# Optimization experiments

Measured on AMD Instinct MI355X. Metric: run time of the kernel, lower is better.

## Reference

```python
import jax, jax.numpy as jnp
import numpy as np

DIM = 2048
H = 16
HD = DIM // H  # 128
EPS = 1e-6


def _rmsnorm(x, w):
    # x: [b, s, d] (float32 math, matches torch RMSNorm .float())
    return x * jax.lax.rsqrt(jnp.mean(x * x, axis=-1, keepdims=True) + EPS) * w


def _rope(x, freqs):
    # x: [b, s, d]; freqs: [s, HD//2, 2] (real, imag) -- complex multiply per pair
    b, s, d = x.shape
    xp = x.reshape(b, s, H, HD // 2, 2)
    xr, xi = xp[..., 0], xp[..., 1]
    fr = freqs[None, :, None, :, 0]
    fi = freqs[None, :, None, :, 1]
    out = jnp.stack([xr * fr - xi * fi, xr * fi + xi * fr], axis=-1)
    return out.reshape(b, s, d)


def _attn(q, k, v):
    # q: [b, sq, d], k/v: [b, skv, d] -> standard SDPA over H heads
    b, sq, d = q.shape
    skv = k.shape[1]
    qh = q.reshape(b, sq, H, HD)
    kh = k.reshape(b, skv, H, HD)
    vh = v.reshape(b, skv, H, HD)
    scores = jnp.einsum('bqhd,bkhd->bhqk', qh, kh) / np.sqrt(HD).astype(np.float32)
    p = jax.nn.softmax(scores, axis=-1)
    out = jnp.einsum('bhqk,bkhd->bqhd', p, vh)
    return out.reshape(b, sq, d)


def _linear(x, w, bias):
    # torch Linear convention: w [out, in]
    return jnp.einsum('bsi,oi->bso', x, w) + bias


def setup_inputs() -> dict:
    key = jax.random.key(0)
    ks = jax.random.split(key, 24)
    rn = lambda k, sh, s=1.0: jax.random.normal(k, sh, dtype=jnp.float32) * s
    B, SX, SC, SR = 2, 2048, 512, 512
    W = 0.02
    return {
        'x': rn(ks[0], (B, SX, DIM)),
        'cam_emb': rn(ks[1], (B, SC, DIM)),
        'render_emb': rn(ks[2], (B, SR, DIM)),
        'freqs_x': rn(ks[3], (SX, HD // 2, 2)),
        'freqs_cam': rn(ks[4], (SC, HD // 2, 2)),
        'freqs_render': rn(ks[5], (SR, HD // 2, 2)),
        'wq': rn(ks[6], (DIM, DIM), W), 'bq': jnp.zeros((DIM,), jnp.float32),
        'wk': rn(ks[7], (DIM, DIM), W), 'bk': jnp.zeros((DIM,), jnp.float32),
        'wv': rn(ks[8], (DIM, DIM), W), 'bv': jnp.zeros((DIM,), jnp.float32),
        'wkr': rn(ks[9], (DIM, DIM), W), 'bkr': jnp.zeros((DIM,), jnp.float32),
        'wvr': rn(ks[10], (DIM, DIM), W), 'bvr': jnp.zeros((DIM,), jnp.float32),
        'wo': rn(ks[11], (DIM, DIM), W), 'bo': jnp.zeros((DIM,), jnp.float32),
        'gq': jnp.ones((DIM,), jnp.float32),
        'gk': jnp.ones((DIM,), jnp.float32),
    }


def reference(x, cam_emb, render_emb, freqs_x, freqs_cam, freqs_render,
              wq, bq, wk, bk, wv, bv, wkr, bkr, wvr, bvr, wo, bo, gq, gk):
    q = _rope(_rmsnorm(_linear(x, wq, bq), gq), freqs_x)
    k_cam = _rope(_rmsnorm(_linear(cam_emb, wk, bk), gk), freqs_cam)
    k_ren = _rope(_rmsnorm(_linear(render_emb, wkr, bkr), gk), freqs_render)
    v_cam = _linear(cam_emb, wv, bv)
    v_ren = _linear(render_emb, wvr, bvr)
    k = jnp.concatenate([k_cam, k_ren], axis=1)
    v = jnp.concatenate([v_cam, v_ren], axis=1)
    out = _attn(q, k, v)
    return _linear(out, wo, bo)
```

## Files before the change

### kernel.cpp

```cpp
#include <hip/hip_runtime.h>

typedef short bf16x8 __attribute__((ext_vector_type(8)));
typedef float f32x4 __attribute__((ext_vector_type(4)));
typedef unsigned short ushort_t;
typedef unsigned int uint_t;

#define DIM 2048
#define NH 16
#define HD 128

__device__ __forceinline__ ushort_t f2b(float f) {
    union { float f; uint_t u; } a; a.f = f;
    uint_t u = a.u;
    return (ushort_t)((u + 0x7fffu + ((u >> 16) & 1u)) >> 16);
}

__device__ __forceinline__ uint_t cvt_pk_bf16(float lo, float hi) {
    uint_t r;
    asm("v_cvt_pk_bf16_f32 %0, %1, %2" : "=v"(r) : "v"(lo), "v"(hi));
    return r;
}

__device__ __forceinline__ void gload_lds16(const void* g, void* l) {
    void* gg = const_cast<void*>(g);
    __builtin_amdgcn_global_load_lds(
        (__attribute__((address_space(1))) uint_t*)gg,
        (__attribute__((address_space(3))) uint_t*)l, 16, 0, 0);
}

struct CvtWArgs { const float* s[6]; };
__global__ __launch_bounds__(256) void k_cvtw(CvtWArgs a, ushort_t* __restrict__ dst) {
    int y = blockIdx.y;
    const float* in = a.s[y];
    ushort_t* out = dst + (size_t)y * 4194304;
    int idx = (blockIdx.x * 256 + threadIdx.x) * 8;
    float4 p = *(const float4*)(in + idx);
    float4 q = *(const float4*)(in + idx + 4);
    uint4 o;
    o.x = (uint_t)f2b(p.x) | ((uint_t)f2b(p.y) << 16);
    o.y = (uint_t)f2b(p.z) | ((uint_t)f2b(p.w) << 16);
    o.z = (uint_t)f2b(q.x) | ((uint_t)f2b(q.y) << 16);
    o.w = (uint_t)f2b(q.z) | ((uint_t)f2b(q.w) << 16);
    *(uint4*)(out + idx) = o;
}

struct Cvt3Args { const float* s[3]; ushort_t* d[3]; int n[3]; };
__global__ __launch_bounds__(256) void k_cvt3(Cvt3Args a) {
    int y = blockIdx.y;
    int idx = (blockIdx.x * 256 + threadIdx.x) * 8;
    if (idx >= a.n[y]) return;
    const float* in = a.s[y];
    ushort_t* out = a.d[y];
    float4 p = *(const float4*)(in + idx);
    float4 q = *(const float4*)(in + idx + 4);
    uint4 o;
    o.x = (uint_t)f2b(p.x) | ((uint_t)f2b(p.y) << 16);
    o.y = (uint_t)f2b(p.z) | ((uint_t)f2b(p.w) << 16);
    o.z = (uint_t)f2b(q.x) | ((uint_t)f2b(q.y) << 16);
    o.w = (uint_t)f2b(q.z) | ((uint_t)f2b(q.w) << 16);
    *(uint4*)(out + idx) = o;
}

struct G8 {
    const ushort_t* A;
    const ushort_t* B;
    const float* bias0;
    const float* bias1;
    void* out0;
    void* out1;
};

template<int MODE>
__global__ __launch_bounds__(512, 2) void k_g256(G8 p0, G8 p1, G8 p2) {
    extern __shared__ __align__(16) char sm[];
    int tid = threadIdx.x, lane = tid & 63, w = tid >> 6;
    int c = lane & 15, g = lane >> 4;
    int wr = w >> 2, wc = w & 3;

    int flat = blockIdx.x;
    G8 ar;
    int bm, bn, vOut = 0;
    if (MODE == 1) {
        int re = (flat & 7) * 32 + (flat >> 3);
        if (re < 128) { ar = p0; bm = re & 15; bn = re >> 4; }
        else {
            int r2 = re - 128;
            int z = r2 >> 6; r2 &= 63;
            ar = z ? p2 : p1;
            bm = r2 & 3; bn = r2 >> 2;
            vOut = (bn >= 8);
        }
    } else {
        int re = (flat & 7) * 16 + (flat >> 3);
        ar = p0; bm = re >> 3; bn = re & 7;
    }

    int wj0 = 2 * w, wj1 = 2 * w + 1;
    int l3 = lane >> 3;
    int swz = ((lane & 7) ^ l3) << 4;
    int RA0 = (wj0 >> 3) * 128 + (wj0 & 7) * 8 + l3;
    int RA1 = (wj1 >> 3) * 128 + (wj1 & 7) * 8 + l3;
    int RB0 = (wj0 >> 2) * 64 + (wj0 & 3) * 8 + l3;
    int RB1 = (wj1 >> 2) * 64 + (wj1 & 3) * 8 + l3;
    const char* sA0 = (const char*)ar.A + (size_t)(bm * 256 + RA0) * 4096 + swz;
    const char* sA1 = (const char*)ar.A + (size_t)(bm * 256 + RA1) * 4096 + swz;
    const char* sB0 = (const char*)ar.B + (size_t)(bn * 256 + RB0) * 4096 + swz;
    const char* sB1 = (const char*)ar.B + (size_t)(bn * 256 + RB1) * 4096 + swz;
    char* dA0 = sm + wj0 * 1024;
    char* dA1 = sm + wj1 * 1024;
    char* dB0 = sm + 32768 + wj0 * 1024;
    char* dB1 = sm + 32768 + wj1 * 1024;

    auto SA = [&](int buf, int half, int t) {
        gload_lds16(sA0 + (size_t)half * 262144 + t * 128, dA0 + buf + half * 16384);
        gload_lds16(sA1 + (size_t)half * 262144 + t * 128, dA1 + buf + half * 16384);
    };
    auto SB = [&](int buf, int half, int t) {
        gload_lds16(sB0 + (size_t)half * 131072 + t * 128, dB0 + buf + half * 16384);
        gload_lds16(sB1 + (size_t)half * 131072 + t * 128, dB1 + buf + half * 16384);
    };

    int bKS0 = (g << 4) ^ ((c & 7) << 4);
    int bKS1 = (64 | (g << 4)) ^ ((c & 7) << 4);
    int aoffL = wr * 8192 + c * 128;
    int boffL = 32768 + wc * 4096 + c * 128;

    f32x4 acc[8][4];
#pragma unroll
    for (int m = 0; m < 8; m++)
#pragma unroll
        for (int n = 0; n < 4; n++) acc[m][n] = (f32x4){0.f, 0.f, 0.f, 0.f};

    bf16x8 aF[4][2], bF0[2][2], bF1[2][2];

    auto RA = [&](int buf, int mh) {
#pragma unroll
        for (int m = 0; m < 4; m++) {
            aF[m][0] = *(const bf16x8*)(sm + buf + mh * 16384 + aoffL + m * 2048 + bKS0);
            aF[m][1] = *(const bf16x8*)(sm + buf + mh * 16384 + aoffL + m * 2048 + bKS1);
        }
    };
    auto RB = [&](int buf, int nh, bf16x8 (&bF)[2][2]) {
#pragma unroll
        for (int n = 0; n < 2; n++) {
            bF[n][0] = *(const bf16x8*)(sm + buf + boffL + nh * 16384 + n * 2048 + bKS0);
            bF[n][1] = *(const bf16x8*)(sm + buf + boffL + nh * 16384 + n * 2048 + bKS1);
        }
    };
    auto MF = [&](int mh, int nh, bf16x8 (&bF)[2][2]) {
        __builtin_amdgcn_s_setprio(1);
#pragma unroll
        for (int m = 0; m < 4; m++)
#pragma unroll
            for (int n = 0; n < 2; n++)
#pragma unroll
                for (int ks = 0; ks < 2; ks++)
                    acc[mh * 4 + m][nh * 2 + n] = __builtin_amdgcn_mfma_f32_16x16x32_bf16(
                        aF[m][ks], bF[n][ks], acc[mh * 4 + m][nh * 2 + n], 0, 0, 0);
        __builtin_amdgcn_s_setprio(0);
    };

    SA(0, 0, 0); SB(0, 0, 0); SA(0, 1, 0); SB(0, 1, 0);
    SA(65536, 0, 1); SB(65536, 0, 1);
    asm volatile("s_waitcnt vmcnt(8)" ::: "memory");
    __builtin_amdgcn_s_barrier();

#pragma unroll 1
    for (int i = 0; i < 16; ++i) {
        int Tb  = 2 * i + 1;
        int Ta2 = (2 * i + 2 > 31) ? 31 : 2 * i + 2;
        int Tb2 = (2 * i + 3 > 31) ? 31 : 2 * i + 3;
        RA(0, 0); RB(0, 0, bF0);
        SA(65536, 1, Tb);
        __builtin_amdgcn_s_barrier();
        MF(0, 0, bF0);
        asm volatile("s_waitcnt vmcnt(6)" ::: "memory");
        __builtin_amdgcn_s_barrier();
        RB(0, 1, bF1);
        SB(65536, 1, Tb);
        __builtin_amdgcn_s_barrier();
        MF(0, 1, bF1);
        __builtin_amdgcn_s_barrier();
        RA(0, 1);
        SA(0, 0, Ta2);
        __builtin_amdgcn_s_barrier();
        MF(1, 0, bF0);
        __builtin_amdgcn_s_barrier();
        SB(0, 0, Ta2);
        __builtin_amdgcn_s_barrier();
        MF(1, 1, bF1);
        asm volatile("s_waitcnt vmcnt(8)" ::: "memory");
        __builtin_amdgcn_s_barrier();
        RA(65536, 0); RB(65536, 0, bF0);
        SA(0, 1, Ta2);
        __builtin_amdgcn_s_barrier();
        MF(0, 0, bF0);
        asm volatile("s_waitcnt vmcnt(6)" ::: "memory");
        __builtin_amdgcn_s_barrier();
        RB(65536, 1, bF1);
        SB(0, 1, Ta2);
        __builtin_amdgcn_s_barrier();
        MF(0, 1, bF1);
        __builtin_amdgcn_s_barrier();
        RA(65536, 1);
        SA(65536, 0, Tb2);
        __builtin_amdgcn_s_barrier();
        MF(1, 0, bF0);
        __builtin_amdgcn_s_barrier();
        SB(65536, 0, Tb2);
        __builtin_amdgcn_s_barrier();
        MF(1, 1, bF1);
        asm volatile("s_waitcnt vmcnt(8)" ::: "memory");
        __builtin_amdgcn_s_barrier();
    }

    int orow0 = bm * 256 + wr * 128 + g * 4;
    int ocol0 = bn * 256 + wc * 64 + c;
    if (MODE == 0 || !vOut) {
        float* o0 = (float*)ar.out0;
#pragma unroll
        for (int n = 0; n < 4; n++) {
            int col = ocol0 + n * 16;
            float bv = ar.bias0[col];
#pragma unroll
            for (int m = 0; m < 8; m++)
#pragma unroll
                for (int q = 0; q < 4; q++)
                    o0[(size_t)(orow0 + m * 16 + q) * 2048 + col] = acc[m][n][q] + bv;
        }
    } else {
        ushort_t* o1 = (ushort_t*)ar.out1;
#pragma unroll
        for (int n = 0; n < 4; n++) {
            int col = ocol0 + n * 16 - 2048;
            float bv = ar.bias1[col];
#pragma unroll
            for (int m = 0; m < 8; m++)
#pragma unroll
                for (int q = 0; q < 4; q++)
                    o1[(size_t)(orow0 + m * 16 + q) * 2048 + col] = f2b(acc[m][n][q] + bv);
        }
    }
}

template<int MERGED>
__global__ __launch_bounds__(512, 2) void k_gemm4(G8 p0, G8 p1, G8 p2) {
    __shared__ __align__(16) char sm[32768];
    int tid = threadIdx.x, lane = tid & 63, w = tid >> 6;
    int c = lane & 15, g = lane >> 4;
    int wr = w >> 2, wc = w & 3;

    int flat = blockIdx.x;
    G8 ar;
    int bm, bn;
    {
        int re = (flat & 7) * 64 + (flat >> 3);
        bm = re & 31; bn = re >> 5;
        ar = p0;
    }

    int chunk = ((tid & 3) ^ ((tid >> 3) & 3)) << 4;
    int r = tid >> 2;
    const char* gA = (const char*)ar.A + (size_t)(bm * 128 + r) * 4096 + chunk;
    const char* gB = (const char*)ar.B + (size_t)(bn * 128 + r) * 4096 + chunk;
    char* wA = sm + w * 1024;
    char* wB = sm + 8192 + w * 1024;

    f32x4 acc[4][2];
#pragma unroll
    for (int m = 0; m < 4; m++)
#pragma unroll
        for (int n = 0; n < 2; n++) acc[m][n] = (f32x4){0.f, 0.f, 0.f, 0.f};

    gload_lds16(gA, wA);
    gload_lds16(gB, wB);
    gload_lds16(gA + 64, wA + 16384);
    gload_lds16(gB + 64, wB + 16384);
    asm volatile("s_waitcnt vmcnt(2)" ::: "memory");
    __builtin_amdgcn_s_barrier();

    int arow = wr * 64 + c;
    int aoff = arow * 64 + ((g ^ ((arow >> 1) & 3)) << 4);
    int brow = wc * 32 + c;
    int boff = 8192 + brow * 64 + ((g ^ ((brow >> 1) & 3)) << 4);

    for (int kt = 0; kt < 64; ++kt) {
        int dboff = (kt & 1) * 16384;
        bf16x8 aF[4], bF[2];
#pragma unroll
        for (int m = 0; m < 4; m++) aF[m] = *(const bf16x8*)(sm + dboff + aoff + m * 1024);
#pragma unroll
        for (int n = 0; n < 2; n++) bF[n] = *(const bf16x8*)(sm + dboff + boff + n * 1024);
        asm volatile("s_waitcnt lgkmcnt(0)" ::: "memory");
        __builtin_amdgcn_sched_barrier(0);
        __builtin_amdgcn_s_barrier();
        int nt = kt + 2; if (nt > 63) nt = 63;
        size_t koff = (size_t)nt * 64;
        __builtin_amdgcn_s_setprio(1);
#pragma unroll
        for (int m = 0; m < 4; m++)
            acc[m][0] = __builtin_amdgcn_mfma_f32_16x16x32_bf16(aF[m], bF[0], acc[m][0], 0, 0, 0);
        gload_lds16(gA + koff, wA + dboff);
#pragma unroll
        for (int m = 0; m < 4; m++)
            acc[m][1] = __builtin_amdgcn_mfma_f32_16x16x32_bf16(aF[m], bF[1], acc[m][1], 0, 0, 0);
        gload_lds16(gB + koff, wB + dboff);
        __builtin_amdgcn_s_setprio(0);
        asm volatile("s_waitcnt vmcnt(2)" ::: "memory");
        __builtin_amdgcn_s_barrier();
    }

    int orow = bm * 128 + wr * 64 + g * 4;
    int ocolb = bn * 128 + wc * 32 + c;
    float* o0 = (float*)ar.out0;
#pragma unroll
    for (int n = 0; n < 2; n++) {
        int ocol = ocolb + n * 16;
        float bv = ar.bias0[ocol];
#pragma unroll
        for (int m = 0; m < 4; m++)
#pragma unroll
            for (int q = 0; q < 4; q++)
                o0[(size_t)(orow + m * 16 + q) * 2048 + ocol] = acc[m][n][q] + bv;
    }
}

__global__ __launch_bounds__(256) void k_rms_rope(const float* __restrict__ in,
                                                  const float* __restrict__ gain,
                                                  const float* __restrict__ freqs,
                                                  ushort_t* __restrict__ out,
                                                  int S, float oscale) {
    int row = blockIdx.x;
    int s = row % S;
    int tid = threadIdx.x;
    const float* p = in + (size_t)row * DIM + tid * 8;
    float4 a = *(const float4*)p;
    float4 b = *(const float4*)(p + 4);
    float y[8] = {a.x, a.y, a.z, a.w, b.x, b.y, b.z, b.w};
    float ss = 0.f;
#pragma unroll
    for (int j = 0; j < 8; j++) ss += y[j] * y[j];
#pragma unroll
    for (int off = 32; off > 0; off >>= 1) ss += __shfl_xor(ss, off, 64);
    __shared__ float red[4];
    int lane = tid & 63, wid = tid >> 6;
    if (lane == 0) red[wid] = ss;
    __syncthreads();
    float tot = red[0] + red[1] + red[2] + red[3];
    float inv = rsqrtf(tot * (1.0f / DIM) + 1e-6f);
    const float* g = gain + tid * 8;
    float4 g0 = *(const float4*)g;
    float4 g1 = *(const float4*)(g + 4);
    float gg[8] = {g0.x, g0.y, g0.z, g0.w, g1.x, g1.y, g1.z, g1.w};
    int p0 = (tid * 8 & 127) >> 1;
    const float* fq = freqs + ((size_t)s * 64 + p0) * 2;
    uint_t ow[4];
#pragma unroll
    for (int j = 0; j < 4; j++) {
        float fr = fq[j * 2 + 0], fi = fq[j * 2 + 1];
        float xr = y[2 * j] * inv * gg[2 * j];
        float xi = y[2 * j + 1] * inv * gg[2 * j + 1];
        float o0 = (xr * fr - xi * fi) * oscale;
        float o1 = (xr * fi + xi * fr) * oscale;
        ow[j] = (uint_t)f2b(o0) | ((uint_t)f2b(o1) << 16);
    }
    *(uint4*)(out + (size_t)row * DIM + tid * 8) = make_uint4(ow[0], ow[1], ow[2], ow[3]);
}

__global__ __launch_bounds__(256) void k_vt(const ushort_t* __restrict__ vcam,
                                            const ushort_t* __restrict__ vren,
                                            ushort_t* __restrict__ vt) {
    __shared__ ushort_t t[64 * 136];
    int kt = blockIdx.x, h = blockIdx.y, b = blockIdx.z;
    int kv0 = kt * 64;
    const ushort_t* src = (kv0 < 512)
        ? vcam + ((size_t)(b * 512 + kv0)) * DIM + h * HD
        : vren + ((size_t)(b * 512 + kv0 - 512)) * DIM + h * HD;
    int tid = threadIdx.x;
#pragma unroll
    for (int i = 0; i < 4; i++) {
        int idx = i * 256 + tid;
        int kv = idx >> 4, c8 = idx & 15;
        uint4 v = *(const uint4*)(src + (size_t)kv * DIM + c8 * 8);
        *(uint4*)(t + kv * 136 + c8 * 8) = v;
    }
    __syncthreads();
    ushort_t* dst = vt + ((size_t)((b * NH + h) * HD)) * 1024 + kv0;
#pragma unroll
    for (int i = 0; i < 4; i++) {
        int idx = i * 256 + tid;
        int d = idx >> 3, c8 = idx & 7;
        ushort_t tmp[8];
#pragma unroll
        for (int j = 0; j < 8; j++) tmp[j] = t[(c8 * 8 + j) * 136 + d];
        uint4 o;
        o.x = (uint_t)tmp[0] | ((uint_t)tmp[1] << 16);
        o.y = (uint_t)tmp[2] | ((uint_t)tmp[3] << 16);
        o.z = (uint_t)tmp[4] | ((uint_t)tmp[5] << 16);
        o.w = (uint_t)tmp[6] | ((uint_t)tmp[7] << 16);
        *(uint4*)(dst + (size_t)d * 1024 + c8 * 8) = o;
    }
}

__global__ __launch_bounds__(512, 4) void k_attn(const ushort_t* __restrict__ Q,
                                                 const ushort_t* __restrict__ Kc,
                                                 const ushort_t* __restrict__ Kr,
                                                 const ushort_t* __restrict__ Vt,
                                                 ushort_t* __restrict__ O) {
    __shared__ __align__(16) char sm[65536];
    int tid = threadIdx.x, lane = tid & 63, w = tid >> 6;
    int c = lane & 15, g = lane >> 4;

    int bid = blockIdx.x;
    int xcd = bid & 7, idx = bid >> 3;
    int combo = idx & 3, qt = idx >> 2;
    int b = combo >> 1, h = xcd * 2 + (combo & 1);

    const ushort_t* qg = Q + ((size_t)(b * 2048 + qt * 128 + w * 16 + c)) * DIM + h * HD + g * 8;
    bf16x8 aQ[4];
#pragma unroll
    for (int ks = 0; ks < 4; ks++) aQ[ks] = *(const bf16x8*)(qg + ks * 32);

    int kbase[4], vbase[8];
#pragma unroll
    for (int n = 0; n < 4; n++) {
        int row = ((n >> 1) << 5) + ((c >> 2) << 3) + ((n & 1) << 2) + (c & 3);
        int sw = (row & 3) | (((row >> 3) & 3) << 2);
        kbase[n] = row * 256 + ((g ^ sw) << 4);
    }
#pragma unroll
    for (int dt = 0; dt < 8; dt++) {
        int vrow = dt * 16 + c;
        vbase[dt] = vrow * 128 + ((g ^ (vrow & 7)) << 4);
    }

    int swk = (lane >> 4) | ((w & 3) << 2);
    size_t klo = (size_t)(8 * w + (lane >> 4)) * 4096 + (size_t)(((lane & 15) ^ swk) << 4);
    size_t vlo = (size_t)(16 * w + (lane >> 3)) * 2048 + (size_t)(((lane & 7) ^ (lane >> 3)) << 4);
    int dst0 = w * 2048;

    const char* kc0 = (const char*)Kc + ((size_t)(b * 512) * DIM + h * HD) * 2;
    const char* kr0 = (const char*)Kr + ((size_t)(b * 512) * DIM + h * HD) * 2;
    const char* vtb = (const char*)Vt + ((size_t)((b * NH + h) * HD)) * 2048;

    float mr = -1e30f, lr = 0.f;
    f32x4 o[8];
#pragma unroll
    for (int d = 0; d < 8; d++) o[d] = (f32x4){0, 0, 0, 0};

    auto STAGE = [&](int DB, int t) {
        const char* kg = (t < 8) ? kc0 + (size_t)t * 262144 : kr0 + (size_t)(t - 8) * 262144;
        const char* vg = vtb + (size_t)t * 128;
        gload_lds16(kg + klo, sm + DB + dst0);
        gload_lds16(kg + klo + 16384, sm + DB + dst0 + 1024);
        gload_lds16(vg + vlo, sm + DB + 16384 + dst0);
        gload_lds16(vg + vlo + 16384, sm + DB + 16384 + dst0 + 1024);
    };

    auto TILE = [&](int DB) {
        f32x4 sT[4];
#pragma unroll
        for (int n = 0; n < 4; n++) sT[n] = (f32x4){0, 0, 0, 0};
#pragma unroll
        for (int n = 0; n < 4; n++)
#pragma unroll
            for (int ks = 0; ks < 4; ks++) {
                bf16x8 aK = *(const bf16x8*)(sm + DB + (kbase[n] ^ (ks << 6)));
                sT[n] = __builtin_amdgcn_mfma_f32_16x16x32_bf16(aK, aQ[ks], sT[n], 0, 0, 0);
            }
        float mloc = sT[0][0];
#pragma unroll
        for (int n = 0; n < 4; n++)
#pragma unroll
            for (int r = 0; r < 4; r++) mloc = fmaxf(mloc, sT[n][r]);
        mloc = fmaxf(mloc, __shfl_xor(mloc, 16, 64));
        mloc = fmaxf(mloc, __shfl_xor(mloc, 32, 64));
        if (!__all(mloc - mr <= 8.0f)) {
            float mn = fmaxf(mr, mloc);
            float al = exp2f(mr - mn);
            mr = mn;
            lr *= al;
#pragma unroll
            for (int d = 0; d < 8; d++) o[d] *= al;
        }
        float p[4][4];
        float ps = 0.f;
#pragma unroll
        for (int n = 0; n < 4; n++)
#pragma unroll
            for (int r = 0; r < 4; r++) {
                p[n][r] = exp2f(sT[n][r] - mr);
                ps += p[n][r];
            }
        ps += __shfl_xor(ps, 16, 64);
        ps += __shfl_xor(ps, 32, 64);
        lr += ps;
#pragma unroll
        for (int kk = 0; kk < 2; kk++) {
            union { uint_t u[4]; bf16x8 v; } bP;
            bP.u[0] = cvt_pk_bf16(p[2 * kk][0], p[2 * kk][1]);
            bP.u[1] = cvt_pk_bf16(p[2 * kk][2], p[2 * kk][3]);
            bP.u[2] = cvt_pk_bf16(p[2 * kk + 1][0], p[2 * kk + 1][1]);
            bP.u[3] = cvt_pk_bf16(p[2 * kk + 1][2], p[2 * kk + 1][3]);
#pragma unroll
            for (int dt = 0; dt < 8; dt++) {
                bf16x8 aV = *(const bf16x8*)(sm + DB + 16384 + (vbase[dt] ^ (kk << 6)));
                o[dt] = __builtin_amdgcn_mfma_f32_16x16x32_bf16(aV, bP.v, o[dt], 0, 0, 0);
            }
        }
    };

    STAGE(0, 0);
    __syncthreads();
#pragma unroll 1
    for (int t = 0; t < 16; t += 2) {
        STAGE(32768, t + 1);
        TILE(0);
        __syncthreads();
        if (t < 14) STAGE(0, t + 2);
        TILE(32768);
        __syncthreads();
    }

    float inv = 1.0f / lr;
    ushort_t* lO = (ushort_t*)sm;
#pragma unroll
    for (int dt = 0; dt < 8; dt++) {
        uint2 wv;
        wv.x = (uint_t)f2b(o[dt][0] * inv) | ((uint_t)f2b(o[dt][1] * inv) << 16);
        wv.y = (uint_t)f2b(o[dt][2] * inv) | ((uint_t)f2b(o[dt][3] * inv) << 16);
        *(uint2*)(lO + (w * 16 + c) * 136 + dt * 16 + g * 4) = wv;
    }
    __syncthreads();
    int row = tid >> 2, c8 = tid & 3;
    const ushort_t* src = lO + row * 136 + c8 * 32;
    ushort_t* dst = O + (size_t)(b * 2048 + qt * 128 + row) * DIM + h * HD + c8 * 32;
#pragma unroll
    for (int k = 0; k < 4; k++) *(uint4*)(dst + k * 8) = *(const uint4*)(src + k * 8);
}

extern "C" void kernel_launch(void* const* d_in, const int* in_sizes, int n_in,
                              void* d_out, int out_size, void* d_ws, size_t ws_size,
                              hipStream_t stream) {
    const float* x   = (const float*)d_in[0];
    const float* cam = (const float*)d_in[1];
    const float* ren = (const float*)d_in[2];
    const float* fx  = (const float*)d_in[3];
    const float* fc  = (const float*)d_in[4];
    const float* fr  = (const float*)d_in[5];
    const float* wq  = (const float*)d_in[6];
    const float* bq  = (const float*)d_in[7];
    const float* wk  = (const float*)d_in[8];
    const float* bk  = (const float*)d_in[9];
    const float* wv  = (const float*)d_in[10];
    const float* bv  = (const float*)d_in[11];
    const float* wkr = (const float*)d_in[12];
    const float* bkr = (const float*)d_in[13];
    const float* wvr = (const float*)d_in[14];
    const float* bvr = (const float*)d_in[15];
    const float* wo  = (const float*)d_in[16];
    const float* bo  = (const float*)d_in[17];
    const float* gq  = (const float*)d_in[18];
    const float* gk  = (const float*)d_in[19];

    char* ws = (char*)d_ws;
    ushort_t* wq_b     = (ushort_t*)(ws + 0);
    ushort_t* wk_b     = (ushort_t*)(ws + 8388608);
    ushort_t* wkr_b    = (ushort_t*)(ws + 25165824);
    ushort_t* wo_b     = (ushort_t*)(ws + 41943040);
    ushort_t* xb       = (ushort_t*)(ws + 50331648);
    ushort_t* camb     = (ushort_t*)(ws + 67108864);
    ushort_t* renb     = (ushort_t*)(ws + 71303168);
    float*    kcam_lin = (float*)(ws + 75497472);
    float*    kren_lin = (float*)(ws + 83886080);
    ushort_t* q_bf     = (ushort_t*)(ws + 92274688);
    ushort_t* kcam_bf  = (ushort_t*)(ws + 109051904);
    ushort_t* kren_bf  = (ushort_t*)(ws + 113246208);
    ushort_t* vcam_bf  = (ushort_t*)(ws + 117440512);
    ushort_t* vren_bf  = (ushort_t*)(ws + 121634816);
    ushort_t* vt       = (ushort_t*)(ws + 75497472);
    ushort_t* attn_bf  = (ushort_t*)(ws + 50331648);
    float*    q_lin    = (float*)d_out;

    hipFuncSetAttribute(reinterpret_cast<const void*>(&k_g256<1>),
                        hipFuncAttributeMaxDynamicSharedMemorySize, 131072);

    CvtWArgs cw{{wq, wk, wv, wkr, wvr, wo}};
    k_cvtw<<<dim3(2048, 6), 256, 0, stream>>>(cw, wq_b);
    Cvt3Args c3{{x, cam, ren}, {xb, camb, renb}, {8388608, 2097152, 2097152}};
    k_cvt3<<<dim3(4096, 3), 256, 0, stream>>>(c3);

    G8 qa{xb, wq_b, bq, nullptr, (void*)q_lin, nullptr};
    G8 kva0{camb, wk_b, bk, bv, (void*)kcam_lin, (void*)vcam_bf};
    G8 kva1{renb, wkr_b, bkr, bvr, (void*)kren_lin, (void*)vren_bf};
    k_g256<1><<<dim3(256, 1, 1), 512, 131072, stream>>>(qa, kva0, kva1);

    k_rms_rope<<<4096, 256, 0, stream>>>(q_lin, gq, fx, q_bf, 2048,
                                         0.08838834764831845f * 1.4426950408889634f);
    k_rms_rope<<<1024, 256, 0, stream>>>(kcam_lin, gk, fc, kcam_bf, 512, 1.0f);
    k_rms_rope<<<1024, 256, 0, stream>>>(kren_lin, gk, fr, kren_bf, 512, 1.0f);
    k_vt<<<dim3(16, 16, 2), 256, 0, stream>>>(vcam_bf, vren_bf, vt);

    k_attn<<<dim3(512, 1, 1), 512, 0, stream>>>(q_bf, kcam_bf, kren_bf, vt, attn_bf);

    G8 oa{attn_bf, wo_b, bo, nullptr, d_out, nullptr};
    k_gemm4<0><<<dim3(512, 1, 1), 512, 0, stream>>>(oa, oa, oa);
}
```

Measured before the change: 229.5 us.

## Fuse V transpose into GEMM epilogue, bf16 intermediates, merge rms-rope, new output GEMM

The projection GEMM now writes Q/K intermediates in bf16 instead of fp32. It also writes V directly in the transposed per-head tile layout, which removes the separate transpose kernel. The three RMSNorm+RoPE launches are merged into one kernel that emits head-major Q/K, so attention uses contiguous per-head loads. Attention now defers the cross-lane reductions of the row max and sum, and the output projection switches to a 128x256-tile, deeper-pipelined GEMM. The cost is bf16 rounding of the pre-norm activations, which adds some numerical error.

```diff
diff --git a/kernel.cpp b/kernel.cpp
--- a/kernel.cpp
+++ b/kernel.cpp
@@ -13,6 +13,11 @@
     union { float f; uint_t u; } a; a.f = f;
     uint_t u = a.u;
     return (ushort_t)((u + 0x7fffu + ((u >> 16) & 1u)) >> 16);
+}
+
+__device__ __forceinline__ float b2f(ushort_t s) {
+    union { uint_t u; float f; } a; a.u = ((uint_t)s) << 16;
+    return a.f;
 }
 
 __device__ __forceinline__ uint_t cvt_pk_bf16(float lo, float hi) {
@@ -70,7 +75,6 @@
     void* out1;
 };
 
-template<int MODE>
 __global__ __launch_bounds__(512, 2) void k_g256(G8 p0, G8 p1, G8 p2) {
     extern __shared__ __align__(16) char sm[];
     int tid = threadIdx.x, lane = tid & 63, w = tid >> 6;
@@ -79,8 +83,8 @@
 
     int flat = blockIdx.x;
     G8 ar;
-    int bm, bn, vOut = 0;
-    if (MODE == 1) {
+    int bm, bn, isKV = 0, kvoff = 0;
+    {
         int re = (flat & 7) * 32 + (flat >> 3);
         if (re < 128) { ar = p0; bm = re & 15; bn = re >> 4; }
         else {
@@ -88,11 +92,8 @@
             int z = r2 >> 6; r2 &= 63;
             ar = z ? p2 : p1;
             bm = r2 & 3; bn = r2 >> 2;
-            vOut = (bn >= 8);
-        }
-    } else {
-        int re = (flat & 7) * 16 + (flat >> 3);
-        ar = p0; bm = re >> 3; bn = re & 7;
+            isKV = 1; kvoff = z ? 512 : 0;
+        }
     }
 
     int wj0 = 2 * w, wj1 = 2 * w + 1;
@@ -216,8 +217,8 @@
 
     int orow0 = bm * 256 + wr * 128 + g * 4;
     int ocol0 = bn * 256 + wc * 64 + c;
-    if (MODE == 0 || !vOut) {
-        float* o0 = (float*)ar.out0;
+    if (!isKV || ocol0 < 2048) {
+        ushort_t* o0 = (ushort_t*)ar.out0;
 #pragma unroll
         for (int n = 0; n < 4; n++) {
             int col = ocol0 + n * 16;
@@ -226,117 +227,190 @@
             for (int m = 0; m < 8; m++)
 #pragma unroll
                 for (int q = 0; q < 4; q++)
-                    o0[(size_t)(orow0 + m * 16 + q) * 2048 + col] = acc[m][n][q] + bv;
+                    o0[(size_t)(orow0 + m * 16 + q) * 2048 + col] = f2b(acc[m][n][q] + bv);
         }
     } else {
         ushort_t* o1 = (ushort_t*)ar.out1;
 #pragma unroll
         for (int n = 0; n < 4; n++) {
-            int col = ocol0 + n * 16 - 2048;
-            float bv = ar.bias1[col];
-#pragma unroll
-            for (int m = 0; m < 8; m++)
-#pragma unroll
-                for (int q = 0; q < 4; q++)
-                    o1[(size_t)(orow0 + m * 16 + q) * 2048 + col] = f2b(acc[m][n][q] + bv);
-        }
-    }
-}
-
-template<int MERGED>
-__global__ __launch_bounds__(512, 2) void k_gemm4(G8 p0, G8 p1, G8 p2) {
-    __shared__ __align__(16) char sm[32768];
+            int col2 = ocol0 + n * 16 - 2048;
+            int h = col2 >> 7, d = col2 & 127;
+            float bv = ar.bias1[col2];
+#pragma unroll
+            for (int m = 0; m < 8; m++) {
+                int r = orow0 + m * 16;
+                int bb = r >> 9;
+                int kvg = kvoff + (r & 511);
+                int t = kvg >> 6, ki = kvg & 63;
+                uint2 wv;
+                wv.x = cvt_pk_bf16(acc[m][n][0] + bv, acc[m][n][1] + bv);
+                wv.y = cvt_pk_bf16(acc[m][n][2] + bv, acc[m][n][3] + bv);
+                *(uint2*)(o1 + (size_t)(((bb * 16 + h) * 16 + t)) * 8192 + d * 64 + ki) = wv;
+            }
+        }
+    }
+}
+
+__global__ __launch_bounds__(512, 2) void k_g128(G8 p0) {
+    extern __shared__ __align__(16) char sm[];
     int tid = threadIdx.x, lane = tid & 63, w = tid >> 6;
     int c = lane & 15, g = lane >> 4;
     int wr = w >> 2, wc = w & 3;
 
     int flat = blockIdx.x;
-    G8 ar;
-    int bm, bn;
-    {
-        int re = (flat & 7) * 64 + (flat >> 3);
-        bm = re & 31; bn = re >> 5;
-        ar = p0;
-    }
-
-    int chunk = ((tid & 3) ^ ((tid >> 3) & 3)) << 4;
-    int r = tid >> 2;
-    const char* gA = (const char*)ar.A + (size_t)(bm * 128 + r) * 4096 + chunk;
-    const char* gB = (const char*)ar.B + (size_t)(bn * 128 + r) * 4096 + chunk;
-    char* wA = sm + w * 1024;
-    char* wB = sm + 8192 + w * 1024;
-
-    f32x4 acc[4][2];
+    int re = (flat & 7) * 32 + (flat >> 3);
+    int bm = re & 31, bn = re >> 5;
+    G8 ar = p0;
+
+    int l3 = lane >> 3;
+    int swz = ((lane & 7) ^ l3) << 4;
+    int wj0 = 2 * w, wj1 = 2 * w + 1;
+    int RB0 = (wj0 >> 2) * 64 + (wj0 & 3) * 8 + l3;
+    int RB1 = (wj1 >> 2) * 64 + (wj1 & 3) * 8 + l3;
+    const char* sA  = (const char*)ar.A + (size_t)(bm * 128 + w * 8 + l3) * 4096 + swz;
+    const char* sB0 = (const char*)ar.B + (size_t)(bn * 256 + RB0) * 4096 + swz;
+    const char* sB1 = (const char*)ar.B + (size_t)(bn * 256 + RB1) * 4096 + swz;
+    char* dA  = sm + w * 1024;
+    char* dB0 = sm + 16384 + wj0 * 1024;
+    char* dB1 = sm + 16384 + wj1 * 1024;
+
+    auto SA = [&](int buf, int half, int t) {
+        gload_lds16(sA + (size_t)half * 262144 + t * 128, dA + buf + half * 8192);
+    };
+    auto SB = [&](int buf, int half, int t) {
+        gload_lds16(sB0 + (size_t)half * 131072 + t * 128, dB0 + buf + half * 16384);
+        gload_lds16(sB1 + (size_t)half * 131072 + t * 128, dB1 + buf + half * 16384);
+    };
+
+    int bKS0 = (g << 4) ^ ((c & 7) << 4);
+    int bKS1 = (64 | (g << 4)) ^ ((c & 7) << 4);
+    int aoffL = wr * 8192 + c * 128;
+    int boffL = 16384 + wc * 4096 + c * 128;
+
+    f32x4 acc[4][4];
 #pragma unroll
     for (int m = 0; m < 4; m++)
 #pragma unroll
-        for (int n = 0; n < 2; n++) acc[m][n] = (f32x4){0.f, 0.f, 0.f, 0.f};
-
-    gload_lds16(gA, wA);
-    gload_lds16(gB, wB);
-    gload_lds16(gA + 64, wA + 16384);
-    gload_lds16(gB + 64, wB + 16384);
-    asm volatile("s_waitcnt vmcnt(2)" ::: "memory");
+        for (int n = 0; n < 4; n++) acc[m][n] = (f32x4){0.f, 0.f, 0.f, 0.f};
+
+    bf16x8 aF[2][2], bF0[2][2], bF1[2][2];
+
+    auto RA = [&](int buf, int mhp) {
+#pragma unroll
+        for (int m = 0; m < 2; m++) {
+            aF[m][0] = *(const bf16x8*)(sm + buf + aoffL + (mhp * 2 + m) * 2048 + bKS0);
+            aF[m][1] = *(const bf16x8*)(sm + buf + aoffL + (mhp * 2 + m) * 2048 + bKS1);
+        }
+    };
+    auto RB = [&](int buf, int nh, bf16x8 (&bF)[2][2]) {
+#pragma unroll
+        for (int n = 0; n < 2; n++) {
+            bF[n][0] = *(const bf16x8*)(sm + buf + boffL + nh * 16384 + n * 2048 + bKS0);
+            bF[n][1] = *(const bf16x8*)(sm + buf + boffL + nh * 16384 + n * 2048 + bKS1);
+        }
+    };
+    auto MF = [&](int mhp, int nh, bf16x8 (&bF)[2][2]) {
+        __builtin_amdgcn_s_setprio(1);
+#pragma unroll
+        for (int m = 0; m < 2; m++)
+#pragma unroll
+            for (int n = 0; n < 2; n++)
+#pragma unroll
+                for (int ks = 0; ks < 2; ks++)
+                    acc[mhp * 2 + m][nh * 2 + n] = __builtin_amdgcn_mfma_f32_16x16x32_bf16(
+                        aF[m][ks], bF[n][ks], acc[mhp * 2 + m][nh * 2 + n], 0, 0, 0);
+        __builtin_amdgcn_s_setprio(0);
+    };
+
+    const int B1 = 49152;
+    SA(0, 0, 0); SA(0, 1, 0); SB(0, 0, 0); SB(0, 1, 0);
+    SA(B1, 0, 1);
+    asm volatile("s_waitcnt vmcnt(1)" ::: "memory");
     __builtin_amdgcn_s_barrier();
 
-    int arow = wr * 64 + c;
-    int aoff = arow * 64 + ((g ^ ((arow >> 1) & 3)) << 4);
-    int brow = wc * 32 + c;
-    int boff = 8192 + brow * 64 + ((g ^ ((brow >> 1) & 3)) << 4);
-
-    for (int kt = 0; kt < 64; ++kt) {
-        int dboff = (kt & 1) * 16384;
-        bf16x8 aF[4], bF[2];
-#pragma unroll
-        for (int m = 0; m < 4; m++) aF[m] = *(const bf16x8*)(sm + dboff + aoff + m * 1024);
-#pragma unroll
-        for (int n = 0; n < 2; n++) bF[n] = *(const bf16x8*)(sm + dboff + boff + n * 1024);
-        asm volatile("s_waitcnt lgkmcnt(0)" ::: "memory");
-        __builtin_amdgcn_sched_barrier(0);
-        __builtin_amdgcn_s_barrier();
-        int nt = kt + 2; if (nt > 63) nt = 63;
-        size_t koff = (size_t)nt * 64;
-        __builtin_amdgcn_s_setprio(1);
+#pragma unroll 1
+    for (int i = 0; i < 16; ++i) {
+        int Tb  = 2 * i + 1;
+        int Ta2 = (2 * i + 2 > 31) ? 31 : 2 * i + 2;
+        int Tb2 = (2 * i + 3 > 31) ? 31 : 2 * i + 3;
+        RA(0, 0); RB(0, 0, bF0);
+        SA(B1, 1, Tb);
+        __builtin_amdgcn_s_barrier();
+        MF(0, 0, bF0);
+        __builtin_amdgcn_s_barrier();
+        RB(0, 1, bF1);
+        SB(B1, 0, Tb);
+        __builtin_amdgcn_s_barrier();
+        MF(0, 1, bF1);
+        __builtin_amdgcn_s_barrier();
+        RA(0, 1);
+        SB(B1, 1, Tb);
+        __builtin_amdgcn_s_barrier();
+        MF(1, 0, bF0);
+        __builtin_amdgcn_s_barrier();
+        SA(0, 0, Ta2);
+        __builtin_amdgcn_s_barrier();
+        MF(1, 1, bF1);
+        asm volatile("s_waitcnt vmcnt(3)" ::: "memory");
+        __builtin_amdgcn_s_barrier();
+        RA(B1, 0); RB(B1, 0, bF0);
+        SA(0, 1, Ta2);
+        __builtin_amdgcn_s_barrier();
+        MF(0, 0, bF0);
+        asm volatile("s_waitcnt vmcnt(2)" ::: "memory");
+        __builtin_amdgcn_s_barrier();
+        RB(B1, 1, bF1);
+        SB(0, 0, Ta2);
+        __builtin_amdgcn_s_barrier();
+        MF(0, 1, bF1);
+        __builtin_amdgcn_s_barrier();
+        RA(B1, 1);
+        SB(0, 1, Ta2);
+        __builtin_amdgcn_s_barrier();
+        MF(1, 0, bF0);
+        __builtin_amdgcn_s_barrier();
+        SA(B1, 0, Tb2);
+        __builtin_amdgcn_s_barrier();
+        MF(1, 1, bF1);
+        asm volatile("s_waitcnt vmcnt(1)" ::: "memory");
+        __builtin_amdgcn_s_barrier();
+    }
+
+    int orow0 = bm * 128 + wr * 64 + g * 4;
+    int ocol0 = bn * 256 + wc * 64 + c;
+    float* o0 = (float*)ar.out0;
+#pragma unroll
+    for (int n = 0; n < 4; n++) {
+        int col = ocol0 + n * 16;
+        float bv = ar.bias0[col];
 #pragma unroll
         for (int m = 0; m < 4; m++)
-            acc[m][0] = __builtin_amdgcn_mfma_f32_16x16x32_bf16(aF[m], bF[0], acc[m][0], 0, 0, 0);
-        gload_lds16(gA + koff, wA + dboff);
-#pragma unroll
-        for (int m = 0; m < 4; m++)
-            acc[m][1] = __builtin_amdgcn_mfma_f32_16x16x32_bf16(aF[m], bF[1], acc[m][1], 0, 0, 0);
-        gload_lds16(gB + koff, wB + dboff);
-        __builtin_amdgcn_s_setprio(0);
-        asm volatile("s_waitcnt vmcnt(2)" ::: "memory");
-        __builtin_amdgcn_s_barrier();
-    }
-
-    int orow = bm * 128 + wr * 64 + g * 4;
-    int ocolb = bn * 128 + wc * 32 + c;
-    float* o0 = (float*)ar.out0;
-#pragma unroll
-    for (int n = 0; n < 2; n++) {
-        int ocol = ocolb + n * 16;
-        float bv = ar.bias0[ocol];
-#pragma unroll
-        for (int m = 0; m < 4; m++)
 #pragma unroll
             for (int q = 0; q < 4; q++)
-                o0[(size_t)(orow + m * 16 + q) * 2048 + ocol] = acc[m][n][q] + bv;
-    }
-}
-
-__global__ __launch_bounds__(256) void k_rms_rope(const float* __restrict__ in,
-                                                  const float* __restrict__ gain,
-                                                  const float* __restrict__ freqs,
-                                                  ushort_t* __restrict__ out,
-                                                  int S, float oscale) {
-    int row = blockIdx.x;
-    int s = row % S;
+                o0[(size_t)(orow0 + m * 16 + q) * 2048 + col] = acc[m][n][q] + bv;
+    }
+}
+
+struct RR { const ushort_t* in; const float* gain; const float* freqs; ushort_t* out; int lgS; float scale; };
+__global__ __launch_bounds__(256) void k_rr(RR a0, RR a1, RR a2) {
+    int bid = blockIdx.x;
+    RR a; int row;
+    if (bid < 4096) { a = a0; row = bid; }
+    else if (bid < 5120) { a = a1; row = bid - 4096; }
+    else { a = a2; row = bid - 5120; }
+    int S = 1 << a.lgS;
+    int s = row & (S - 1);
+    int b = row >> a.lgS;
     int tid = threadIdx.x;
-    const float* p = in + (size_t)row * DIM + tid * 8;
-    float4 a = *(const float4*)p;
-    float4 b = *(const float4*)(p + 4);
-    float y[8] = {a.x, a.y, a.z, a.w, b.x, b.y, b.z, b.w};
+    uint4 v = *(const uint4*)(a.in + (size_t)row * 2048 + tid * 8);
+    ushort_t us[8];
+    us[0] = (ushort_t)(v.x & 0xffff); us[1] = (ushort_t)(v.x >> 16);
+    us[2] = (ushort_t)(v.y & 0xffff); us[3] = (ushort_t)(v.y >> 16);
+    us[4] = (ushort_t)(v.z & 0xffff); us[5] = (ushort_t)(v.z >> 16);
+    us[6] = (ushort_t)(v.w & 0xffff); us[7] = (ushort_t)(v.w >> 16);
+    float y[8];
+#pragma unroll
+    for (int j = 0; j < 8; j++) y[j] = b2f(us[j]);
     float ss = 0.f;
 #pragma unroll
     for (int j = 0; j < 8; j++) ss += y[j] * y[j];
@@ -348,58 +422,25 @@
     __syncthreads();
     float tot = red[0] + red[1] + red[2] + red[3];
     float inv = rsqrtf(tot * (1.0f / DIM) + 1e-6f);
-    const float* g = gain + tid * 8;
-    float4 g0 = *(const float4*)g;
-    float4 g1 = *(const float4*)(g + 4);
+    const float* gp = a.gain + tid * 8;
+    float4 g0 = *(const float4*)gp;
+    float4 g1 = *(const float4*)(gp + 4);
     float gg[8] = {g0.x, g0.y, g0.z, g0.w, g1.x, g1.y, g1.z, g1.w};
     int p0 = (tid * 8 & 127) >> 1;
-    const float* fq = freqs + ((size_t)s * 64 + p0) * 2;
+    const float* fq = a.freqs + ((size_t)s * 64 + p0) * 2;
     uint_t ow[4];
 #pragma unroll
     for (int j = 0; j < 4; j++) {
         float fr = fq[j * 2 + 0], fi = fq[j * 2 + 1];
         float xr = y[2 * j] * inv * gg[2 * j];
         float xi = y[2 * j + 1] * inv * gg[2 * j + 1];
-        float o0 = (xr * fr - xi * fi) * oscale;
-        float o1 = (xr * fi + xi * fr) * oscale;
+        float o0 = (xr * fr - xi * fi) * a.scale;
+        float o1 = (xr * fi + xi * fr) * a.scale;
         ow[j] = (uint_t)f2b(o0) | ((uint_t)f2b(o1) << 16);
     }
-    *(uint4*)(out + (size_t)row * DIM + tid * 8) = make_uint4(ow[0], ow[1], ow[2], ow[3]);
-}
-
-__global__ __launch_bounds__(256) void k_vt(const ushort_t* __restrict__ vcam,
-                                            const ushort_t* __restrict__ vren,
-                                            ushort_t* __restrict__ vt) {
-    __shared__ ushort_t t[64 * 136];
-    int kt = blockIdx.x, h = blockIdx.y, b = blockIdx.z;
-    int kv0 = kt * 64;
-    const ushort_t* src = (kv0 < 512)
-        ? vcam + ((size_t)(b * 512 + kv0)) * DIM + h * HD
-        : vren + ((size_t)(b * 512 + kv0 - 512)) * DIM + h * HD;
-    int tid = threadIdx.x;
-#pragma unroll
-    for (int i = 0; i < 4; i++) {
-        int idx = i * 256 + tid;
-        int kv = idx >> 4, c8 = idx & 15;
-        uint4 v = *(const uint4*)(src + (size_t)kv * DIM + c8 * 8);
-        *(uint4*)(t + kv * 136 + c8 * 8) = v;
-    }
-    __syncthreads();
-    ushort_t* dst = vt + ((size_t)((b * NH + h) * HD)) * 1024 + kv0;
-#pragma unroll
-    for (int i = 0; i < 4; i++) {
-        int idx = i * 256 + tid;
-        int d = idx >> 3, c8 = idx & 7;
-        ushort_t tmp[8];
-#pragma unroll
-        for (int j = 0; j < 8; j++) tmp[j] = t[(c8 * 8 + j) * 136 + d];
-        uint4 o;
-        o.x = (uint_t)tmp[0] | ((uint_t)tmp[1] << 16);
-        o.y = (uint_t)tmp[2] | ((uint_t)tmp[3] << 16);
-        o.z = (uint_t)tmp[4] | ((uint_t)tmp[5] << 16);
-        o.w = (uint_t)tmp[6] | ((uint_t)tmp[7] << 16);
-        *(uint4*)(dst + (size_t)d * 1024 + c8 * 8) = o;
-    }
+    int h = tid >> 4;
+    ushort_t* dst = a.out + ((size_t)((b * 16 + h) * S + s)) * 128 + (tid & 15) * 8;
+    *(uint4*)dst = make_uint4(ow[0], ow[1], ow[2], ow[3]);
 }
 
 __global__ __launch_bounds__(512, 4) void k_attn(const ushort_t* __restrict__ Q,
@@ -415,8 +456,9 @@
     int xcd = bid & 7, idx = bid >> 3;
     int combo = idx & 3, qt = idx >> 2;
     int b = combo >> 1, h = xcd * 2 + (combo & 1);
-
-    const ushort_t* qg = Q + ((size_t)(b * 2048 + qt * 128 + w * 16 + c)) * DIM + h * HD + g * 8;
+    int bh = b * 16 + h;
+
+    const ushort_t* qg = Q + ((size_t)(bh * 2048 + qt * 128 + w * 16 + c)) * 128 + g * 8;
     bf16x8 aQ[4];
 #pragma unroll
     for (int ks = 0; ks < 4; ks++) aQ[ks] = *(const bf16x8*)(qg + ks * 32);
@@ -435,13 +477,13 @@
     }
 
     int swk = (lane >> 4) | ((w & 3) << 2);
-    size_t klo = (size_t)(8 * w + (lane >> 4)) * 4096 + (size_t)(((lane & 15) ^ swk) << 4);
-    size_t vlo = (size_t)(16 * w + (lane >> 3)) * 2048 + (size_t)(((lane & 7) ^ (lane >> 3)) << 4);
+    int klo = (8 * w + (lane >> 4)) * 256 + (((lane & 15) ^ swk) << 4);
+    int vlo = (16 * w + (lane >> 3)) * 128 + (((lane & 7) ^ (lane >> 3)) << 4);
     int dst0 = w * 2048;
 
-    const char* kc0 = (const char*)Kc + ((size_t)(b * 512) * DIM + h * HD) * 2;
-    const char* kr0 = (const char*)Kr + ((size_t)(b * 512) * DIM + h * HD) * 2;
-    const char* vtb = (const char*)Vt + ((size_t)((b * NH + h) * HD)) * 2048;
+    const char* kcb = (const char*)Kc + (size_t)bh * 131072;
+    const char* krb = (const char*)Kr + (size_t)bh * 131072;
+    const char* vtb = (const char*)Vt + (size_t)bh * 262144;
 
     float mr = -1e30f, lr = 0.f;
     f32x4 o[8];
@@ -449,12 +491,12 @@
     for (int d = 0; d < 8; d++) o[d] = (f32x4){0, 0, 0, 0};
 
     auto STAGE = [&](int DB, int t) {
-        const char* kg = (t < 8) ? kc0 + (size_t)t * 262144 : kr0 + (size_t)(t - 8) * 262144;
-        const char* vg = vtb + (size_t)t * 128;
+        const char* kg = (t < 8) ? kcb + t * 16384 : krb + (t - 8) * 16384;
+        const char* vg = vtb + t * 16384;
         gload_lds16(kg + klo, sm + DB + dst0);
-        gload_lds16(kg + klo + 16384, sm + DB + dst0 + 1024);
+        gload_lds16(kg + klo + 1024, sm + DB + dst0 + 1024);
         gload_lds16(vg + vlo, sm + DB + 16384 + dst0);
-        gload_lds16(vg + vlo + 16384, sm + DB + 16384 + dst0 + 1024);
+        gload_lds16(vg + vlo + 1024, sm + DB + 16384 + dst0 + 1024);
     };
 
     auto TILE = [&](int DB) {
@@ -473,10 +515,10 @@
         for (int n = 0; n < 4; n++)
 #pragma unroll
             for (int r = 0; r < 4; r++) mloc = fmaxf(mloc, sT[n][r]);
-        mloc = fmaxf(mloc, __shfl_xor(mloc, 16, 64));
-        mloc = fmaxf(mloc, __shfl_xor(mloc, 32, 64));
         if (!__all(mloc - mr <= 8.0f)) {
-            float mn = fmaxf(mr, mloc);
+            float mx = fmaxf(mloc, __shfl_xor(mloc, 16, 64));
+            mx = fmaxf(mx, __shfl_xor(mx, 32, 64));
+            float mn = fmaxf(mr, mx);
             float al = exp2f(mr - mn);
             mr = mn;
             lr *= al;
@@ -492,8 +534,6 @@
                 p[n][r] = exp2f(sT[n][r] - mr);
                 ps += p[n][r];
             }
-        ps += __shfl_xor(ps, 16, 64);
-        ps += __shfl_xor(ps, 32, 64);
         lr += ps;
 #pragma unroll
         for (int kk = 0; kk < 2; kk++) {
@@ -522,6 +562,8 @@
         __syncthreads();
     }
 
+    lr += __shfl_xor(lr, 16, 64);
+    lr += __shfl_xor(lr, 32, 64);
     float inv = 1.0f / lr;
     ushort_t* lO = (ushort_t*)sm;
 #pragma unroll
@@ -534,7 +576,7 @@
     __syncthreads();
     int row = tid >> 2, c8 = tid & 3;
     const ushort_t* src = lO + row * 136 + c8 * 32;
-    ushort_t* dst = O + (size_t)(b * 2048 + qt * 128 + row) * DIM + h * HD + c8 * 32;
+    ushort_t* dst = O + (size_t)(b * 2048 + qt * 128 + row) * 2048 + h * 128 + c8 * 32;
 #pragma unroll
     for (int k = 0; k < 4; k++) *(uint4*)(dst + k * 8) = *(const uint4*)(src + k * 8);
 }
@@ -571,19 +613,19 @@
     ushort_t* xb       = (ushort_t*)(ws + 50331648);
     ushort_t* camb     = (ushort_t*)(ws + 67108864);
     ushort_t* renb     = (ushort_t*)(ws + 71303168);
-    float*    kcam_lin = (float*)(ws + 75497472);
-    float*    kren_lin = (float*)(ws + 83886080);
+    ushort_t* kcam_lin = (ushort_t*)(ws + 75497472);
+    ushort_t* kren_lin = (ushort_t*)(ws + 79691776);
+    ushort_t* vt       = (ushort_t*)(ws + 83886080);
     ushort_t* q_bf     = (ushort_t*)(ws + 92274688);
     ushort_t* kcam_bf  = (ushort_t*)(ws + 109051904);
     ushort_t* kren_bf  = (ushort_t*)(ws + 113246208);
-    ushort_t* vcam_bf  = (ushort_t*)(ws + 117440512);
-    ushort_t* vren_bf  = (ushort_t*)(ws + 121634816);
-    ushort_t* vt       = (ushort_t*)(ws + 75497472);
     ushort_t* attn_bf  = (ushort_t*)(ws + 50331648);
-    float*    q_lin    = (float*)d_out;
-
-    hipFuncSetAttribute(reinterpret_cast<const void*>(&k_g256<1>),
+    ushort_t* q_lin    = (ushort_t*)d_out;
+
+    hipFuncSetAttribute(reinterpret_cast<const void*>(&k_g256),
                         hipFuncAttributeMaxDynamicSharedMemorySize, 131072);
+    hipFuncSetAttribute(reinterpret_cast<const void*>(&k_g128),
+                        hipFuncAttributeMaxDynamicSharedMemorySize, 98304);
 
     CvtWArgs cw{{wq, wk, wv, wkr, wvr, wo}};
     k_cvtw<<<dim3(2048, 6), 256, 0, stream>>>(cw, wq_b);
@@ -591,18 +633,17 @@
     k_cvt3<<<dim3(4096, 3), 256, 0, stream>>>(c3);
 
     G8 qa{xb, wq_b, bq, nullptr, (void*)q_lin, nullptr};
-    G8 kva0{camb, wk_b, bk, bv, (void*)kcam_lin, (void*)vcam_bf};
-    G8 kva1{renb, wkr_b, bkr, bvr, (void*)kren_lin, (void*)vren_bf};
-    k_g256<1><<<dim3(256, 1, 1), 512, 131072, stream>>>(qa, kva0, kva1);
-
-    k_rms_rope<<<4096, 256, 0, stream>>>(q_lin, gq, fx, q_bf, 2048,
-                                         0.08838834764831845f * 1.4426950408889634f);
-    k_rms_rope<<<1024, 256, 0, stream>>>(kcam_lin, gk, fc, kcam_bf, 512, 1.0f);
-    k_rms_rope<<<1024, 256, 0, stream>>>(kren_lin, gk, fr, kren_bf, 512, 1.0f);
-    k_vt<<<dim3(16, 16, 2), 256, 0, stream>>>(vcam_bf, vren_bf, vt);
+    G8 kva0{camb, wk_b, bk, bv, (void*)kcam_lin, (void*)vt};
+    G8 kva1{renb, wkr_b, bkr, bvr, (void*)kren_lin, (void*)vt};
+    k_g256<<<dim3(256, 1, 1), 512, 131072, stream>>>(qa, kva0, kva1);
+
+    RR r0{q_lin, gq, fx, q_bf, 11, 0.08838834764831845f * 1.4426950408889634f};
+    RR r1{kcam_lin, gk, fc, kcam_bf, 9, 1.0f};
+    RR r2{kren_lin, gk, fr, kren_bf, 9, 1.0f};
+    k_rr<<<dim3(6144, 1, 1), 256, 0, stream>>>(r0, r1, r2);
 
     k_attn<<<dim3(512, 1, 1), 512, 0, stream>>>(q_bf, kcam_bf, kren_bf, vt, attn_bf);
 
     G8 oa{attn_bf, wo_b, bo, nullptr, d_out, nullptr};
-    k_gemm4<0><<<dim3(512, 1, 1), 512, 0, stream>>>(oa, oa, oa);
-}
+    k_g128<<<dim3(256, 1, 1), 512, 98304, stream>>>(oa);
+}
```

New measurement: 212.4 us. -7.4%, faster.
